# Kernel optimization log

Measured on AMD Instinct MI355X. Metric: run time of the kernel, lower is better.

## Reference

```python
import jax, jax.numpy as jnp
import numpy as np

N = 10000      # total nodes
E = 320000     # total edges (avg degree 32)
T = 8          # time steps
F = 32         # feature width (in = hidden = out)
L = 3          # len(hidden_sizes) + 1 layers
EPS = 1e-5     # BatchNorm eps


def setup_inputs() -> dict:
    key = jax.random.key(0)
    ks = jax.random.split(key, 6)
    node_features = jax.random.normal(ks[0], (N, F), dtype=jnp.float32)
    edges_weight = jax.random.uniform(ks[1], (T, E), dtype=jnp.float32)
    src = jax.random.randint(ks[2], (E,), 0, N, dtype=jnp.int32)
    dst = jax.random.randint(ks[3], (E,), 0, N, dtype=jnp.int32)
    Ws = jax.random.normal(ks[4], (L, F, F), dtype=jnp.float32) / np.float32(np.sqrt(F))
    bs = jnp.zeros((L, F), dtype=jnp.float32)
    gammas = jnp.ones((L, F), dtype=jnp.float32)
    betas = jnp.zeros((L, F), dtype=jnp.float32)
    return dict(node_features=node_features, edges_weight=edges_weight,
                src=src, dst=dst, Ws=Ws, bs=bs, gammas=gammas, betas=betas)


def reference(node_features, edges_weight, src, dst, Ws, bs, gammas, betas):
    w_et = edges_weight.T            # (E, T), matches edge_weights.t()
    n = node_features.shape[0]
    h = node_features                # (N, F) first layer, (N, T, F) after
    for l in range(L):
        hs = h[src]                  # gather source-node features
        if hs.ndim == 2:
            hs = hs[:, None, :]      # (E, 1, F) -> broadcast over T
        msg = hs * w_et[:, :, None]  # u_mul_e: (E, T, F)
        agg = jax.ops.segment_sum(msg, dst, num_segments=n)  # sum per dst: (N, T, F)
        out = jnp.einsum('ntf,of->nto', agg, Ws[l]) + bs[l]  # Linear
        # BatchNorm1d (training mode): stats over (N, T) per channel, biased var
        mean = out.mean(axis=(0, 1))
        var = out.var(axis=(0, 1))
        out = (out - mean) * jax.lax.rsqrt(var + EPS) * gammas[l] + betas[l]
        h = jax.nn.relu(out)
    return h                         # (N, T, F)
```

## Files before the change

### kernel.cpp

```cpp
#include <hip/hip_runtime.h>

#define TF 8
#define FD 32
#define EPSV 1e-5f

__device__ __forceinline__ void atomAddF(float* p, float v) {
#if defined(__HIP_PLATFORM_AMD__)
    unsafeAtomicAdd(p, v);
#else
    atomicAdd(p, v);
#endif
}

__device__ __forceinline__ unsigned int f2bfu(float x) {
    unsigned int u = __float_as_uint(x);
    return (u + 0x7FFFu + ((u >> 16) & 1u)) >> 16;
}
__device__ __forceinline__ float bfx(unsigned int w, int hi) {
    return __uint_as_float(hi ? (w & 0xFFFF0000u) : (w << 16));
}

__global__ __launch_bounds__(256) void hist_kernel(
    const int* __restrict__ dst, int* __restrict__ counts, int E)
{
    int e = blockIdx.x * 256 + threadIdx.x;
    if (e < E) atomicAdd(&counts[dst[e]], 1);
}

__global__ __launch_bounds__(1024) void scan_kernel(
    const int* __restrict__ counts, int* __restrict__ rowptr,
    int* __restrict__ cursor, int Nn)
{
    __shared__ int totals[1024];
    int tid = threadIdx.x;
    int per = (Nn + 1023) >> 10;
    int start = tid * per;
    int end = min(start + per, Nn);
    if (end < start) end = start;
    int s = 0;
    for (int i = start; i < end; ++i) s += counts[i];
    totals[tid] = s;
    __syncthreads();
    for (int off = 1; off < 1024; off <<= 1) {
        int t2 = (tid >= off) ? totals[tid - off] : 0;
        __syncthreads();
        totals[tid] += t2;
        __syncthreads();
    }
    int running = totals[tid] - s;
    for (int i = start; i < end; ++i) {
        rowptr[i] = running;
        cursor[i] = running;
        running += counts[i];
    }
    if (tid == 1023) rowptr[Nn] = totals[1023];
}

__global__ __launch_bounds__(256) void fillA_kernel(
    const int* __restrict__ src, const int* __restrict__ dst,
    const float* __restrict__ w, int* __restrict__ cursor,
    int* __restrict__ ssrc, uint4* __restrict__ wsb, int E)
{
    int e = blockIdx.x * 256 + threadIdx.x;
    if (e >= E) return;
    int d = dst[e];
    int j = atomicAdd(&cursor[d], 1);
    ssrc[j] = src[e];
    uint4 p;
    p.x = f2bfu(w[(size_t)0 * E + e]) | (f2bfu(w[(size_t)1 * E + e]) << 16);
    p.y = f2bfu(w[(size_t)2 * E + e]) | (f2bfu(w[(size_t)3 * E + e]) << 16);
    p.z = f2bfu(w[(size_t)4 * E + e]) | (f2bfu(w[(size_t)5 * E + e]) << 16);
    p.w = f2bfu(w[(size_t)6 * E + e]) | (f2bfu(w[(size_t)7 * E + e]) << 16);
    wsb[j] = p;
}

template <int MODE, int OUTB>
__global__ __launch_bounds__(256) void agg_gemm3_kernel(
    const float* __restrict__ hf, const uint4* __restrict__ hb,
    const float* __restrict__ coefIn,
    const int* __restrict__ rowptr, const int* __restrict__ ssrc,
    const uint4* __restrict__ wsb,
    const float* __restrict__ W, const float* __restrict__ bias,
    unsigned int* __restrict__ outU, float* __restrict__ outF,
    float* __restrict__ stats)
{
    __shared__ float Wt[FD * FD];
    __shared__ float red[512];
    __shared__ float pacc[8 * TF * FD];
    int tid = threadIdx.x;
    int slot = tid >> 5, f = tid & 31;
    {
        int ff = tid & 31;
        Wt[ff * FD + (tid >> 5)] = W[tid];
        Wt[ff * FD + ((tid + 256) >> 5)] = W[tid + 256];
        Wt[ff * FD + ((tid + 512) >> 5)] = W[tid + 512];
        Wt[ff * FD + ((tid + 768) >> 5)] = W[tid + 768];
    }
    float cA = 0.f, cB = 0.f;
    if (MODE == 1) { cA = coefIn[f]; cB = coefIn[FD + f]; }

    int node = blockIdx.x;
    int rs = rowptr[node], re = rowptr[node + 1];

    float acc[TF];
    #pragma unroll
    for (int t = 0; t < TF; ++t) acc[t] = 0.f;

    int j = rs + slot;
    int s = (j < re) ? ssrc[j] : 0;
    for (; j < re; j += 8) {
        int jn = j + 8;
        int s_next = (jn < re) ? ssrc[jn] : 0;
        uint4 wp = wsb[j];
        unsigned int ww[4] = { wp.x, wp.y, wp.z, wp.w };
        if (MODE == 0) {
            float hv = hf[(size_t)s * FD + f];
            #pragma unroll
            for (int t = 0; t < TF; ++t)
                acc[t] = fmaf(bfx(ww[t >> 1], t & 1), hv, acc[t]);
        } else {
            uint4 hp = hb[(size_t)s * FD + f];
            unsigned int hw[4] = { hp.x, hp.y, hp.z, hp.w };
            #pragma unroll
            for (int t = 0; t < TF; ++t) {
                float hr = bfx(hw[t >> 1], t & 1);
                float hn = fmaxf(0.f, fmaf(hr, cA, cB));
                acc[t] = fmaf(bfx(ww[t >> 1], t & 1), hn, acc[t]);
            }
        }
        s = s_next;
    }
    #pragma unroll
    for (int t = 0; t < TF; ++t)
        pacc[slot * (TF * FD) + t * FD + f] = acc[t];
    __syncthreads();
    int t2 = tid >> 5;
    float asum = 0.f;
    #pragma unroll
    for (int sl = 0; sl < 8; ++sl)
        asum += pacc[sl * (TF * FD) + t2 * FD + f];
    red[tid] = asum;
    __syncthreads();

    float oval = bias[f];
    #pragma unroll
    for (int k = 0; k < FD; ++k)
        oval = fmaf(red[t2 * FD + k], Wt[k * FD + f], oval);
    if (!OUTB)
        outF[(size_t)node * (TF * FD) + tid] = oval;

    __syncthreads();
    red[tid] = oval;
    red[256 + tid] = oval * oval;
    __syncthreads();
    if (OUTB) {
        if (tid < 128) {
            int ff = tid >> 2, q = tid & 3;
            unsigned int lo = f2bfu(red[(q * 2) * FD + ff]);
            unsigned int hi = f2bfu(red[(q * 2 + 1) * FD + ff]);
            outU[(size_t)node * 128 + ff * 4 + q] = lo | (hi << 16);
        }
        __syncthreads();
    }
    #pragma unroll
    for (int stride = 128; stride >= 32; stride >>= 1) {
        if (tid < stride) {
            red[tid] += red[tid + stride];
            red[256 + tid] += red[256 + tid + stride];
        }
        __syncthreads();
    }
    if (tid < 32) {
        int slot2 = blockIdx.x & 31;
        atomAddF(&stats[slot2 * 64 + tid], red[tid]);
        atomAddF(&stats[slot2 * 64 + 32 + tid], red[256 + tid]);
    }
}

__global__ void finalize_kernel(const float* __restrict__ stats,
                                const float* __restrict__ gamma,
                                const float* __restrict__ beta,
                                float* __restrict__ coef, float inv_count)
{
    int o = threadIdx.x;
    float s = 0.f, sq = 0.f;
    #pragma unroll
    for (int k = 0; k < 32; ++k) { s += stats[k * 64 + o]; sq += stats[k * 64 + 32 + o]; }
    float mean = s * inv_count;
    float var  = sq * inv_count - mean * mean;
    float sc   = gamma[o] * rsqrtf(var + EPSV);
    coef[o]      = sc;
    coef[FD + o] = beta[o] - mean * sc;
}

__global__ __launch_bounds__(256) void norm_relu_kernel(
    float* __restrict__ x, const float* __restrict__ coef, int n4)
{
    int gid = blockIdx.x * 256 + threadIdx.x;
    if (gid >= n4) return;
    float4 v = ((const float4*)x)[gid];
    int o = (gid * 4) & 31;
    float4 r;
    r.x = fmaxf(0.f, fmaf(v.x, coef[o],     coef[32 + o]));
    r.y = fmaxf(0.f, fmaf(v.y, coef[o + 1], coef[33 + o]));
    r.z = fmaxf(0.f, fmaf(v.z, coef[o + 2], coef[34 + o]));
    r.w = fmaxf(0.f, fmaf(v.w, coef[o + 3], coef[35 + o]));
    ((float4*)x)[gid] = r;
}

__global__ __launch_bounds__(256) void scatter0_kernel(
    const float* __restrict__ h, const float* __restrict__ w,
    const int* __restrict__ src, const int* __restrict__ dst,
    float* __restrict__ agg, int E)
{
    int gid = blockIdx.x * 256 + threadIdx.x;
    int e = gid >> 5;
    if (e >= E) return;
    int f = gid & 31;
    int s = src[e], d = dst[e];
    float hv = h[(size_t)s * FD + f];
    float* aggd = agg + (size_t)d * (TF * FD) + f;
    #pragma unroll
    for (int t = 0; t < TF; ++t)
        atomAddF(aggd + t * FD, w[(size_t)t * E + e] * hv);
}

__global__ __launch_bounds__(256) void scatterL_kernel(
    const float* __restrict__ h, const float* __restrict__ w,
    const int* __restrict__ src, const int* __restrict__ dst,
    float* __restrict__ agg, int E)
{
    int gid = blockIdx.x * 256 + threadIdx.x;
    int e = gid >> 5;
    if (e >= E) return;
    int f = gid & 31;
    int s = src[e], d = dst[e];
    const float* hs = h + (size_t)s * (TF * FD) + f;
    float* aggd = agg + (size_t)d * (TF * FD) + f;
    #pragma unroll
    for (int t = 0; t < TF; ++t)
        atomAddF(aggd + t * FD, w[(size_t)t * E + e] * hs[t * FD]);
}

__global__ __launch_bounds__(256) void gemm_stats_kernel(
    const float* __restrict__ agg, const float* __restrict__ W,
    const float* __restrict__ bias, float* __restrict__ out,
    float* __restrict__ stats, int nrows)
{
    __shared__ float Wt[FD * FD];
    __shared__ float rows[8 * FD];
    int tid = threadIdx.x;
    for (int i = tid; i < FD * FD; i += 256) {
        int o = i >> 5, f = i & 31;
        Wt[f * FD + o] = W[i];
    }
    int o = tid & 31;
    int r = tid >> 5;
    float b = bias[o];
    float sum = 0.f, sumsq = 0.f;
    int ngroups = (nrows + 7) >> 3;
    for (int g = blockIdx.x; g < ngroups; g += gridDim.x) {
        int row0 = g * 8;
        __syncthreads();
        int idx = row0 * FD + tid;
        rows[tid] = (idx < nrows * FD) ? agg[idx] : 0.f;
        __syncthreads();
        int row = row0 + r;
        if (row < nrows) {
            float acc = b;
            #pragma unroll
            for (int f2 = 0; f2 < FD; ++f2)
                acc = fmaf(rows[r * FD + f2], Wt[f2 * FD + o], acc);
            out[(size_t)row * FD + o] = acc;
            sum += acc;
            sumsq += acc * acc;
        }
    }
    __syncthreads();
    rows[tid] = sum;
    Wt[tid] = sumsq;
    __syncthreads();
    for (int stride = 128; stride >= 32; stride >>= 1) {
        if (tid < stride) { rows[tid] += rows[tid + stride]; Wt[tid] += Wt[tid + stride]; }
        __syncthreads();
    }
    if (tid < 32) {
        int slot = blockIdx.x & 31;
        atomAddF(&stats[slot * 64 + tid], rows[tid]);
        atomAddF(&stats[slot * 64 + 32 + tid], Wt[tid]);
    }
}

extern "C" void kernel_launch(void* const* d_in, const int* in_sizes, int n_in,
                              void* d_out, int out_size, void* d_ws, size_t ws_size,
                              hipStream_t stream)
{
    const float* nf  = (const float*)d_in[0];
    const float* wgt = (const float*)d_in[1];
    const int*   src = (const int*)d_in[2];
    const int*   dst = (const int*)d_in[3];
    const float* Ws  = (const float*)d_in[4];
    const float* bs  = (const float*)d_in[5];
    const float* gam = (const float*)d_in[6];
    const float* bet = (const float*)d_in[7];

    int E  = in_sizes[2];
    int Nn = in_sizes[0] / FD;
    int nrows = Nn * TF;
    int n4 = nrows * FD / 4;
    float inv_count = 1.0f / (float)nrows;
    float* out = (float*)d_out;

    size_t idxInts = (size_t)(3 * Nn + 4);
    size_t needW = (idxInts + (size_t)E + 4 * (size_t)E + 128 * (size_t)Nn * 2
                    + 3 * 2048 + 3 * 64) * 4;

    int eb = (E + 255) / 256;

    if (ws_size >= needW) {
        int*          counts = (int*)d_ws;
        int*          cursor = counts + Nn;
        int*          rowptr = cursor + Nn;
        int*          ssrc   = counts + idxInts;
        uint4*        wsb    = (uint4*)(ssrc + E);
        unsigned int* hb0    = (unsigned int*)(wsb + E);
        unsigned int* hb1    = hb0 + (size_t)Nn * 128;
        float*        stats  = (float*)(hb1 + (size_t)Nn * 128);
        float*        coef   = stats + 3 * 2048;

        hipMemsetAsync(counts, 0, (size_t)Nn * sizeof(int), stream);
        hipMemsetAsync(stats, 0, 3 * 2048 * sizeof(float), stream);
        hist_kernel<<<eb, 256, 0, stream>>>(dst, counts, E);
        scan_kernel<<<1, 1024, 0, stream>>>(counts, rowptr, cursor, Nn);
        fillA_kernel<<<eb, 256, 0, stream>>>(src, dst, wgt, cursor, ssrc, wsb, E);

        agg_gemm3_kernel<0, 1><<<Nn, 256, 0, stream>>>(
            nf, nullptr, nullptr, rowptr, ssrc, wsb, Ws, bs,
            hb0, nullptr, stats);
        finalize_kernel<<<1, 32, 0, stream>>>(stats, gam, bet, coef, inv_count);
        agg_gemm3_kernel<1, 1><<<Nn, 256, 0, stream>>>(
            nullptr, (const uint4*)hb0, coef, rowptr, ssrc, wsb,
            Ws + FD * FD, bs + FD, hb1, nullptr, stats + 2048);
        finalize_kernel<<<1, 32, 0, stream>>>(
            stats + 2048, gam + FD, bet + FD, coef + 64, inv_count);
        agg_gemm3_kernel<1, 0><<<Nn, 256, 0, stream>>>(
            nullptr, (const uint4*)hb1, coef + 64, rowptr, ssrc, wsb,
            Ws + 2 * FD * FD, bs + 2 * FD, nullptr, out, stats + 2 * 2048);
        finalize_kernel<<<1, 32, 0, stream>>>(
            stats + 2 * 2048, gam + 2 * FD, bet + 2 * FD, coef + 2 * 64, inv_count);
        norm_relu_kernel<<<(n4 + 255) / 256, 256, 0, stream>>>(out, coef + 2 * 64, n4);
    } else {
        float* agg   = (float*)d_ws;
        float* stats = agg + (size_t)nrows * FD;
        float* coef  = stats + 2048;
        int scatterBlocks = (E * 32 + 255) / 256;
        for (int l = 0; l < 3; ++l) {
            hipMemsetAsync(agg, 0, (size_t)nrows * FD * sizeof(float), stream);
            hipMemsetAsync(stats, 0, 2048 * sizeof(float), stream);
            if (l == 0)
                scatter0_kernel<<<scatterBlocks, 256, 0, stream>>>(nf, wgt, src, dst, agg, E);
            else
                scatterL_kernel<<<scatterBlocks, 256, 0, stream>>>(out, wgt, src, dst, agg, E);
            gemm_stats_kernel<<<2048, 256, 0, stream>>>(
                agg, Ws + l * FD * FD, bs + l * FD, out, stats, nrows);
            finalize_kernel<<<1, 32, 0, stream>>>(
                stats, gam + l * FD, bet + l * FD, coef, inv_count);
            norm_relu_kernel<<<(n4 + 255) / 256, 256, 0, stream>>>(out, coef, n4);
        }
    }
}
```

Measured before the change: 251.2 us.

## Fold BN finalize into consumer kernels and unroll edge gather by four

Removes the three single-block finalize launches by having each block of the next aggregation kernel, and the final norm-relu kernel, recompute the BatchNorm scale and shift from the partial stats in shared memory. It also merges the two memsets into one by placing stats next to counts, and unrolls the edge loop so each thread issues four independent index, weight and feature loads per iteration. This trades fewer launches and more memory-level parallelism for redundant per-block stats reductions (32x64 reads per block) and higher register pressure.

```diff
diff --git a/kernel.cpp b/kernel.cpp
--- a/kernel.cpp
+++ b/kernel.cpp
@@ -75,9 +75,10 @@
 }
 
 template <int MODE, int OUTB>
-__global__ __launch_bounds__(256) void agg_gemm3_kernel(
+__global__ __launch_bounds__(256) void agg_gemm4_kernel(
     const float* __restrict__ hf, const uint4* __restrict__ hb,
-    const float* __restrict__ coefIn,
+    const float* __restrict__ statsPrev, const float* __restrict__ gamma,
+    const float* __restrict__ beta, float inv_count,
     const int* __restrict__ rowptr, const int* __restrict__ ssrc,
     const uint4* __restrict__ wsb,
     const float* __restrict__ W, const float* __restrict__ bias,
@@ -87,6 +88,7 @@
     __shared__ float Wt[FD * FD];
     __shared__ float red[512];
     __shared__ float pacc[8 * TF * FD];
+    __shared__ float cf[64];
     int tid = threadIdx.x;
     int slot = tid >> 5, f = tid & 31;
     {
@@ -96,8 +98,22 @@
         Wt[ff * FD + ((tid + 512) >> 5)] = W[tid + 512];
         Wt[ff * FD + ((tid + 768) >> 5)] = W[tid + 768];
     }
+    if (MODE == 1 && tid < 32) {
+        float s = 0.f, sq = 0.f;
+        #pragma unroll
+        for (int k = 0; k < 32; ++k) {
+            s  += statsPrev[k * 64 + tid];
+            sq += statsPrev[k * 64 + 32 + tid];
+        }
+        float mean = s * inv_count;
+        float var  = sq * inv_count - mean * mean;
+        float scv  = gamma[tid] * rsqrtf(var + EPSV);
+        cf[tid]      = scv;
+        cf[32 + tid] = beta[tid] - mean * scv;
+    }
+    __syncthreads();
     float cA = 0.f, cB = 0.f;
-    if (MODE == 1) { cA = coefIn[f]; cB = coefIn[FD + f]; }
+    if (MODE == 1) { cA = cf[f]; cB = cf[32 + f]; }
 
     int node = blockIdx.x;
     int rs = rowptr[node], re = rowptr[node + 1];
@@ -106,30 +122,55 @@
     #pragma unroll
     for (int t = 0; t < TF; ++t) acc[t] = 0.f;
 
-    int j = rs + slot;
-    int s = (j < re) ? ssrc[j] : 0;
-    for (; j < re; j += 8) {
-        int jn = j + 8;
-        int s_next = (jn < re) ? ssrc[jn] : 0;
-        uint4 wp = wsb[j];
-        unsigned int ww[4] = { wp.x, wp.y, wp.z, wp.w };
+    for (int j = rs + slot; j < re; j += 32) {
+        int  jj[4];
+        bool vv[4];
+        jj[0] = j; vv[0] = true;
+        #pragma unroll
+        for (int q = 1; q < 4; ++q) {
+            int jq = j + 8 * q;
+            vv[q] = jq < re;
+            jj[q] = vv[q] ? jq : j;
+        }
+        int sx[4];
+        #pragma unroll
+        for (int q = 0; q < 4; ++q) sx[q] = ssrc[jj[q]];
+        uint4 wq[4];
+        #pragma unroll
+        for (int q = 0; q < 4; ++q) wq[q] = wsb[jj[q]];
+        #pragma unroll
+        for (int q = 1; q < 4; ++q)
+            if (!vv[q]) { wq[q].x = 0u; wq[q].y = 0u; wq[q].z = 0u; wq[q].w = 0u; }
+
         if (MODE == 0) {
-            float hv = hf[(size_t)s * FD + f];
+            float hq[4];
             #pragma unroll
-            for (int t = 0; t < TF; ++t)
-                acc[t] = fmaf(bfx(ww[t >> 1], t & 1), hv, acc[t]);
+            for (int q = 0; q < 4; ++q) hq[q] = hf[(size_t)sx[q] * FD + f];
+            #pragma unroll
+            for (int q = 0; q < 4; ++q) {
+                unsigned int w_[4] = { wq[q].x, wq[q].y, wq[q].z, wq[q].w };
+                #pragma unroll
+                for (int t = 0; t < TF; ++t)
+                    acc[t] = fmaf(bfx(w_[t >> 1], t & 1), hq[q], acc[t]);
+            }
         } else {
-            uint4 hp = hb[(size_t)s * FD + f];
-            unsigned int hw[4] = { hp.x, hp.y, hp.z, hp.w };
+            uint4 pq[4];
             #pragma unroll
-            for (int t = 0; t < TF; ++t) {
-                float hr = bfx(hw[t >> 1], t & 1);
-                float hn = fmaxf(0.f, fmaf(hr, cA, cB));
-                acc[t] = fmaf(bfx(ww[t >> 1], t & 1), hn, acc[t]);
+            for (int q = 0; q < 4; ++q) pq[q] = hb[(size_t)sx[q] * FD + f];
+            #pragma unroll
+            for (int q = 0; q < 4; ++q) {
+                unsigned int w_[4] = { wq[q].x, wq[q].y, wq[q].z, wq[q].w };
+                unsigned int h_[4] = { pq[q].x, pq[q].y, pq[q].z, pq[q].w };
+                #pragma unroll
+                for (int t = 0; t < TF; ++t) {
+                    float hr = bfx(h_[t >> 1], t & 1);
+                    float hn = fmaxf(0.f, fmaf(hr, cA, cB));
+                    acc[t] = fmaf(bfx(w_[t >> 1], t & 1), hn, acc[t]);
+                }
             }
         }
-        s = s_next;
-    }
+    }
+
     #pragma unroll
     for (int t = 0; t < TF; ++t)
         pacc[slot * (TF * FD) + t * FD + f] = acc[t];
@@ -177,6 +218,122 @@
     }
 }
 
+__global__ __launch_bounds__(256) void norm_relu2_kernel(
+    float* __restrict__ x, const float* __restrict__ stats,
+    const float* __restrict__ gamma, const float* __restrict__ beta,
+    float inv_count, int n4)
+{
+    __shared__ float cf[64];
+    int tid = threadIdx.x;
+    if (tid < 32) {
+        float s = 0.f, sq = 0.f;
+        #pragma unroll
+        for (int k = 0; k < 32; ++k) {
+            s  += stats[k * 64 + tid];
+            sq += stats[k * 64 + 32 + tid];
+        }
+        float mean = s * inv_count;
+        float var  = sq * inv_count - mean * mean;
+        float scv  = gamma[tid] * rsqrtf(var + EPSV);
+        cf[tid]      = scv;
+        cf[32 + tid] = beta[tid] - mean * scv;
+    }
+    __syncthreads();
+    int gid = blockIdx.x * 256 + tid;
+    if (gid >= n4) return;
+    float4 v = ((const float4*)x)[gid];
+    int o = (gid * 4) & 31;
+    float4 r;
+    r.x = fmaxf(0.f, fmaf(v.x, cf[o],     cf[32 + o]));
+    r.y = fmaxf(0.f, fmaf(v.y, cf[o + 1], cf[33 + o]));
+    r.z = fmaxf(0.f, fmaf(v.z, cf[o + 2], cf[34 + o]));
+    r.w = fmaxf(0.f, fmaf(v.w, cf[o + 3], cf[35 + o]));
+    ((float4*)x)[gid] = r;
+}
+
+__global__ __launch_bounds__(256) void scatter0_kernel(
+    const float* __restrict__ h, const float* __restrict__ w,
+    const int* __restrict__ src, const int* __restrict__ dst,
+    float* __restrict__ agg, int E)
+{
+    int gid = blockIdx.x * 256 + threadIdx.x;
+    int e = gid >> 5;
+    if (e >= E) return;
+    int f = gid & 31;
+    int s = src[e], d = dst[e];
+    float hv = h[(size_t)s * FD + f];
+    float* aggd = agg + (size_t)d * (TF * FD) + f;
+    #pragma unroll
+    for (int t = 0; t < TF; ++t)
+        atomAddF(aggd + t * FD, w[(size_t)t * E + e] * hv);
+}
+
+__global__ __launch_bounds__(256) void scatterL_kernel(
+    const float* __restrict__ h, const float* __restrict__ w,
+    const int* __restrict__ src, const int* __restrict__ dst,
+    float* __restrict__ agg, int E)
+{
+    int gid = blockIdx.x * 256 + threadIdx.x;
+    int e = gid >> 5;
+    if (e >= E) return;
+    int f = gid & 31;
+    int s = src[e], d = dst[e];
+    const float* hs = h + (size_t)s * (TF * FD) + f;
+    float* aggd = agg + (size_t)d * (TF * FD) + f;
+    #pragma unroll
+    for (int t = 0; t < TF; ++t)
+        atomAddF(aggd + t * FD, w[(size_t)t * E + e] * hs[t * FD]);
+}
+
+__global__ __launch_bounds__(256) void gemm_stats_kernel(
+    const float* __restrict__ agg, const float* __restrict__ W,
+    const float* __restrict__ bias, float* __restrict__ out,
+    float* __restrict__ stats, int nrows)
+{
+    __shared__ float Wt[FD * FD];
+    __shared__ float rows[8 * FD];
+    int tid = threadIdx.x;
+    for (int i = tid; i < FD * FD; i += 256) {
+        int o = i >> 5, f = i & 31;
+        Wt[f * FD + o] = W[i];
+    }
+    int o = tid & 31;
+    int r = tid >> 5;
+    float b = bias[o];
+    float sum = 0.f, sumsq = 0.f;
+    int ngroups = (nrows + 7) >> 3;
+    for (int g = blockIdx.x; g < ngroups; g += gridDim.x) {
+        int row0 = g * 8;
+        __syncthreads();
+        int idx = row0 * FD + tid;
+        rows[tid] = (idx < nrows * FD) ? agg[idx] : 0.f;
+        __syncthreads();
+        int row = row0 + r;
+        if (row < nrows) {
+            float acc = b;
+            #pragma unroll
+            for (int f2 = 0; f2 < FD; ++f2)
+                acc = fmaf(rows[r * FD + f2], Wt[f2 * FD + o], acc);
+            out[(size_t)row * FD + o] = acc;
+            sum += acc;
+            sumsq += acc * acc;
+        }
+    }
+    __syncthreads();
+    rows[tid] = sum;
+    Wt[tid] = sumsq;
+    __syncthreads();
+    for (int stride = 128; stride >= 32; stride >>= 1) {
+        if (tid < stride) { rows[tid] += rows[tid + stride]; Wt[tid] += Wt[tid + stride]; }
+        __syncthreads();
+    }
+    if (tid < 32) {
+        int slot = blockIdx.x & 31;
+        atomAddF(&stats[slot * 64 + tid], rows[tid]);
+        atomAddF(&stats[slot * 64 + 32 + tid], Wt[tid]);
+    }
+}
+
 __global__ void finalize_kernel(const float* __restrict__ stats,
                                 const float* __restrict__ gamma,
                                 const float* __restrict__ beta,
@@ -190,7 +347,7 @@
     float var  = sq * inv_count - mean * mean;
     float sc   = gamma[o] * rsqrtf(var + EPSV);
     coef[o]      = sc;
-    coef[FD + o] = beta[o] - mean * sc;
+    coef[32 + o] = beta[o] - mean * sc;
 }
 
 __global__ __launch_bounds__(256) void norm_relu_kernel(
@@ -208,89 +365,6 @@
     ((float4*)x)[gid] = r;
 }
 
-__global__ __launch_bounds__(256) void scatter0_kernel(
-    const float* __restrict__ h, const float* __restrict__ w,
-    const int* __restrict__ src, const int* __restrict__ dst,
-    float* __restrict__ agg, int E)
-{
-    int gid = blockIdx.x * 256 + threadIdx.x;
-    int e = gid >> 5;
-    if (e >= E) return;
-    int f = gid & 31;
-    int s = src[e], d = dst[e];
-    float hv = h[(size_t)s * FD + f];
-    float* aggd = agg + (size_t)d * (TF * FD) + f;
-    #pragma unroll
-    for (int t = 0; t < TF; ++t)
-        atomAddF(aggd + t * FD, w[(size_t)t * E + e] * hv);
-}
-
-__global__ __launch_bounds__(256) void scatterL_kernel(
-    const float* __restrict__ h, const float* __restrict__ w,
-    const int* __restrict__ src, const int* __restrict__ dst,
-    float* __restrict__ agg, int E)
-{
-    int gid = blockIdx.x * 256 + threadIdx.x;
-    int e = gid >> 5;
-    if (e >= E) return;
-    int f = gid & 31;
-    int s = src[e], d = dst[e];
-    const float* hs = h + (size_t)s * (TF * FD) + f;
-    float* aggd = agg + (size_t)d * (TF * FD) + f;
-    #pragma unroll
-    for (int t = 0; t < TF; ++t)
-        atomAddF(aggd + t * FD, w[(size_t)t * E + e] * hs[t * FD]);
-}
-
-__global__ __launch_bounds__(256) void gemm_stats_kernel(
-    const float* __restrict__ agg, const float* __restrict__ W,
-    const float* __restrict__ bias, float* __restrict__ out,
-    float* __restrict__ stats, int nrows)
-{
-    __shared__ float Wt[FD * FD];
-    __shared__ float rows[8 * FD];
-    int tid = threadIdx.x;
-    for (int i = tid; i < FD * FD; i += 256) {
-        int o = i >> 5, f = i & 31;
-        Wt[f * FD + o] = W[i];
-    }
-    int o = tid & 31;
-    int r = tid >> 5;
-    float b = bias[o];
-    float sum = 0.f, sumsq = 0.f;
-    int ngroups = (nrows + 7) >> 3;
-    for (int g = blockIdx.x; g < ngroups; g += gridDim.x) {
-        int row0 = g * 8;
-        __syncthreads();
-        int idx = row0 * FD + tid;
-        rows[tid] = (idx < nrows * FD) ? agg[idx] : 0.f;
-        __syncthreads();
-        int row = row0 + r;
-        if (row < nrows) {
-            float acc = b;
-            #pragma unroll
-            for (int f2 = 0; f2 < FD; ++f2)
-                acc = fmaf(rows[r * FD + f2], Wt[f2 * FD + o], acc);
-            out[(size_t)row * FD + o] = acc;
-            sum += acc;
-            sumsq += acc * acc;
-        }
-    }
-    __syncthreads();
-    rows[tid] = sum;
-    Wt[tid] = sumsq;
-    __syncthreads();
-    for (int stride = 128; stride >= 32; stride >>= 1) {
-        if (tid < stride) { rows[tid] += rows[tid + stride]; Wt[tid] += Wt[tid + stride]; }
-        __syncthreads();
-    }
-    if (tid < 32) {
-        int slot = blockIdx.x & 31;
-        atomAddF(&stats[slot * 64 + tid], rows[tid]);
-        atomAddF(&stats[slot * 64 + 32 + tid], Wt[tid]);
-    }
-}
-
 extern "C" void kernel_launch(void* const* d_in, const int* in_sizes, int n_in,
                               void* d_out, int out_size, void* d_ws, size_t ws_size,
                               hipStream_t stream)
@@ -311,44 +385,47 @@
     float inv_count = 1.0f / (float)nrows;
     float* out = (float*)d_out;
 
-    size_t idxInts = (size_t)(3 * Nn + 4);
-    size_t needW = (idxInts + (size_t)E + 4 * (size_t)E + 128 * (size_t)Nn * 2
-                    + 3 * 2048 + 3 * 64) * 4;
+    size_t offCounts = 0;
+    size_t offStats  = offCounts + (size_t)Nn;
+    size_t offCursor = offStats + 3 * 2048;
+    size_t offRowptr = offCursor + (size_t)Nn;
+    size_t offSsrc   = offRowptr + (size_t)Nn + 4;
+    size_t offWsb    = (offSsrc + (size_t)E + 3) & ~(size_t)3;
+    size_t offHb0    = offWsb + 4 * (size_t)E;
+    size_t offHb1    = offHb0 + 128 * (size_t)Nn;
+    size_t needW     = (offHb1 + 128 * (size_t)Nn) * 4;
 
     int eb = (E + 255) / 256;
 
     if (ws_size >= needW) {
-        int*          counts = (int*)d_ws;
-        int*          cursor = counts + Nn;
-        int*          rowptr = cursor + Nn;
-        int*          ssrc   = counts + idxInts;
-        uint4*        wsb    = (uint4*)(ssrc + E);
-        unsigned int* hb0    = (unsigned int*)(wsb + E);
-        unsigned int* hb1    = hb0 + (size_t)Nn * 128;
-        float*        stats  = (float*)(hb1 + (size_t)Nn * 128);
-        float*        coef   = stats + 3 * 2048;
-
-        hipMemsetAsync(counts, 0, (size_t)Nn * sizeof(int), stream);
-        hipMemsetAsync(stats, 0, 3 * 2048 * sizeof(float), stream);
+        int*          base   = (int*)d_ws;
+        int*          counts = base + offCounts;
+        float*        stats  = (float*)(base + offStats);
+        int*          cursor = base + offCursor;
+        int*          rowptr = base + offRowptr;
+        int*          ssrc   = base + offSsrc;
+        uint4*        wsb    = (uint4*)(base + offWsb);
+        unsigned int* hb0    = (unsigned int*)(base + offHb0);
+        unsigned int* hb1    = (unsigned int*)(base + offHb1);
+
+        hipMemsetAsync(counts, 0, ((size_t)Nn + 3 * 2048) * sizeof(int), stream);
         hist_kernel<<<eb, 256, 0, stream>>>(dst, counts, E);
         scan_kernel<<<1, 1024, 0, stream>>>(counts, rowptr, cursor, Nn);
         fillA_kernel<<<eb, 256, 0, stream>>>(src, dst, wgt, cursor, ssrc, wsb, E);
 
-        agg_gemm3_kernel<0, 1><<<Nn, 256, 0, stream>>>(
-            nf, nullptr, nullptr, rowptr, ssrc, wsb, Ws, bs,
-            hb0, nullptr, stats);
-        finalize_kernel<<<1, 32, 0, stream>>>(stats, gam, bet, coef, inv_count);
-        agg_gemm3_kernel<1, 1><<<Nn, 256, 0, stream>>>(
-            nullptr, (const uint4*)hb0, coef, rowptr, ssrc, wsb,
-            Ws + FD * FD, bs + FD, hb1, nullptr, stats + 2048);
-        finalize_kernel<<<1, 32, 0, stream>>>(
-            stats + 2048, gam + FD, bet + FD, coef + 64, inv_count);
-        agg_gemm3_kernel<1, 0><<<Nn, 256, 0, stream>>>(
-            nullptr, (const uint4*)hb1, coef + 64, rowptr, ssrc, wsb,
-            Ws + 2 * FD * FD, bs + 2 * FD, nullptr, out, stats + 2 * 2048);
-        finalize_kernel<<<1, 32, 0, stream>>>(
-            stats + 2 * 2048, gam + 2 * FD, bet + 2 * FD, coef + 2 * 64, inv_count);
-        norm_relu_kernel<<<(n4 + 255) / 256, 256, 0, stream>>>(out, coef + 2 * 64, n4);
+        agg_gemm4_kernel<0, 1><<<Nn, 256, 0, stream>>>(
+            nf, nullptr, nullptr, nullptr, nullptr, inv_count,
+            rowptr, ssrc, wsb, Ws, bs, hb0, nullptr, stats);
+        agg_gemm4_kernel<1, 1><<<Nn, 256, 0, stream>>>(
+            nullptr, (const uint4*)hb0, stats, gam, bet, inv_count,
+            rowptr, ssrc, wsb, Ws + FD * FD, bs + FD, hb1, nullptr,
+            stats + 2048);
+        agg_gemm4_kernel<1, 0><<<Nn, 256, 0, stream>>>(
+            nullptr, (const uint4*)hb1, stats + 2048, gam + FD, bet + FD,
+            inv_count, rowptr, ssrc, wsb, Ws + 2 * FD * FD, bs + 2 * FD,
+            nullptr, out, stats + 2 * 2048);
+        norm_relu2_kernel<<<(n4 + 255) / 256, 256, 0, stream>>>(
+            out, stats + 2 * 2048, gam + 2 * FD, bet + 2 * FD, inv_count, n4);
     } else {
         float* agg   = (float*)d_ws;
         float* stats = agg + (size_t)nrows * FD;
```

Measured after the change: 306.3 us. 21.9% more time.
